# Kernel tuning notes

Measured on AMD Instinct MI355X. Metric: run time of the kernel, lower is better.

## Reference

```python
import jax, jax.numpy as jnp
import numpy as np
import math

B = 2048
INPUT_SIZE = 1024
OUTPUT_SIZE = 512
SPONGE = 1024
ACT = 256
REC = 256
STORE = ACT + REC  # 512
DEPTH = 8
BDEPTH = 10
NEUTRAL_C = 1.0
SQRT2 = math.sqrt(2.0)


def _make_structure():
    # Deterministic stand-in for the module's random.sample-based recall wiring.
    rng = np.random.RandomState(0)
    half = (SPONGE + 1) // 2
    shuffle_perm = np.array([i // 2 + (i % 2) * half for i in range(SPONGE)], dtype=np.int64)
    unused = []
    recall = []
    for i in range(DEPTH):
        unused.extend(range(i * STORE, (i + 1) * STORE))
        sel = rng.choice(len(unused), size=REC, replace=False)
        sel_set = set(sel.tolist())
        recall.append([unused[k] for k in sorted(sel_set)])
        unused = [u for k, u in enumerate(unused) if k not in sel_set]
    out_mem = np.array(sorted(unused), dtype=np.int64)  # 2048 leftover memory columns
    bf_size = len(out_mem) + SPONGE  # 3072
    bf_depth = int(math.ceil(math.log2(bf_size)))  # 12
    bf_half = (bf_size + 1) // 2
    bf_perm = np.array([i // 2 + (i % 2) * bf_half for i in range(bf_size)], dtype=np.int64)
    return shuffle_perm, np.array(recall, dtype=np.int64), out_mem, bf_perm, bf_size, bf_depth


def setup_inputs() -> dict:
    key = jax.random.key(0)
    ks = jax.random.split(key, 6)
    shuffle_perm, recall_idx, out_mem_idx, bf_perm, bf_size, bf_depth = _make_structure()
    return {
        "X": jax.random.normal(ks[0], (B, INPUT_SIZE), jnp.float32),
        "scales": jnp.ones((INPUT_SIZE,), jnp.float32),
        "angles": jax.random.uniform(ks[1], (DEPTH, BDEPTH, SPONGE // 2), jnp.float32) * (2 * math.pi),
        "act_bias": jax.random.normal(ks[2], (DEPTH, ACT), jnp.float32),
        "act_activation": jax.random.normal(ks[3], (DEPTH, ACT), jnp.float32),
        "act_curvature": jax.random.normal(ks[4], (DEPTH, ACT), jnp.float32),
        "bf_angles": jax.random.uniform(ks[5], (bf_depth, bf_size // 2), jnp.float32) * (2 * math.pi),
        "shuffle_perm": jnp.asarray(shuffle_perm),
        "recall_idx": jnp.asarray(recall_idx),
        "output_mem_idx": jnp.asarray(out_mem_idx),
        "bf_perm": jnp.asarray(bf_perm),
    }


def _base_activation(x, c):
    # In the source, `a` is overwritten with torch.tensor(1.0), so a == 1.
    t = (math.pi / 4) / c
    y0 = (1.0 / c) * (1.0 / SQRT2 - math.cos(math.pi / 2))  # = 1/(c*sqrt(2))
    m0 = math.sin(math.pi / 2)  # = 1
    y1 = (1.0 / c) * (1.0 / SQRT2 - 1.0)
    m1 = math.sin(0.0)  # = 0
    mid = (1.0 / c) * (1.0 / SQRT2 - jnp.cos(math.pi / 4 + c * x))
    return jnp.where(x > t, y0 + m0 * (x - t), jnp.where(x < -t, y1 + m1 * (x + t), mid))


def _butterfly(x, angles, perm):
    # angles: [n_layers, exch]; shuffle -> Givens rotation per pair, extra passthrough
    exch = angles.shape[1]
    for j in range(angles.shape[0]):
        s = x[:, perm]
        x1, x2 = s[:, :exch], s[:, exch:2 * exch]
        ca, sa = jnp.cos(angles[j]), jnp.sin(angles[j])
        x = jnp.concatenate([ca * x1 + sa * x2, -sa * x1 + ca * x2, s[:, 2 * exch:]], axis=1)
    return x


def reference(X, scales, angles, act_bias, act_activation, act_curvature, bf_angles,
              shuffle_perm, recall_idx, output_mem_idx, bf_perm):
    Xs = X * scales
    sponge = Xs[:, :SPONGE]  # input_size == sponge_size: no zero pad, memory[0] is empty
    mem = jnp.zeros((Xs.shape[0], DEPTH * STORE), Xs.dtype)
    for i in range(DEPTH):
        sponge = _butterfly(sponge, angles[i], shuffle_perm)
        x1 = sponge[:, STORE:STORE + ACT] + act_bias[i]  # activation_position == store_size
        c = 0.5 * NEUTRAL_C * (act_curvature[i] + jnp.sqrt(act_curvature[i] ** 2 + 1.0))
        ap = _base_activation(x1, c)
        am = _base_activation(-x1, c)
        act_out = jnp.stack([ap, am], axis=2).reshape(ap.shape[0], 2 * ACT)  # interleave +/-
        mem = mem.at[:, i * STORE:(i + 1) * STORE].set(sponge[:, :STORE])
        recall = mem[:, recall_idx[i]]  # indices only address already-filled columns
        # [act_out | sponge[store:act_pos] (empty) | sponge[act_pos+ACT:] | recall]
        sponge = jnp.concatenate([act_out, sponge[:, STORE + ACT:], recall], axis=1)
    pre = jnp.concatenate([mem[:, output_mem_idx], sponge], axis=1)  # [B, 3072]
    out = _butterfly(pre, bf_angles, bf_perm)
    return out[:, :OUTPUT_SIZE]
```

## Files before the change

kernel.cpp:

```cpp
#include <hip/hip_runtime.h>
#include <hip/hip_bf16.h>
#include <math.h>

#define NB 2048
#define DEPTH 8
#define BDEPTH 10
#define BFDEPTH 12

#define N_SPONGE_CS (DEPTH * BDEPTH * 512)
#define N_BF_CS     (BFDEPTH * 1536)
#define TAB_FLOATS  (2 * (N_SPONGE_CS + N_BF_CS))
#define MEM_FLOATS_PER_ROW 4096

__global__ void cs_precompute(const float* __restrict__ angles,
                              const float* __restrict__ bf_angles,
                              float* __restrict__ tab) {
    int i = blockIdx.x * 256 + threadIdx.x;
    float a;
    if (i < N_SPONGE_CS)                a = angles[i];
    else if (i < N_SPONGE_CS + N_BF_CS) a = bf_angles[i - N_SPONGE_CS];
    else return;
    float s, c;
    sincosf(a, &s, &c);
    tab[2 * i]     = c;
    tab[2 * i + 1] = s;
}

__device__ __forceinline__ float base_act(float x, float c, float ic, float tt,
                                          float y0, float y1) {
    float mid = ic * (0.70710678118654752f - __cosf(0.78539816339744831f + c * x));
    return x > tt ? (y0 + (x - tt)) : (x < -tt ? y1 : mid);
}

template <int MEM_LDS>
__launch_bounds__(256, 8)
__global__ void sponge_kernel(const float* __restrict__ X,
                              const float* __restrict__ scales,
                              const float* __restrict__ act_bias,
                              const float* __restrict__ act_curv,
                              const int*   __restrict__ recall_idx,
                              const int*   __restrict__ out_mem_idx,
                              const float* __restrict__ tab,
                              float*       __restrict__ gmem,
                              float*       __restrict__ out) {
    __shared__ float buf[3072];
    __shared__ __hip_bfloat16 memb[MEM_LDS ? 4096 : 2];
    const int t   = threadIdx.x;
    const int row = blockIdx.x;
    float* g = gmem + (size_t)row * MEM_FLOATS_PER_ROW;

    {
        float4 xv = ((const float4*)(X + (size_t)row * 1024))[t];
        float4 sv = ((const float4*)scales)[t];
        ((float4*)buf)[t] = make_float4(xv.x * sv.x, xv.y * sv.y,
                                        xv.z * sv.z, xv.w * sv.w);
    }
    __syncthreads();

    float* cur = buf;
    float* alt = buf + 1024;
    const float* tb = tab;

    for (int d = 0; d < DEPTH; ++d) {
        for (int st = 0; st < BDEPTH; ++st) {
            const float4 cs = *(const float4*)(tb + 4 * t);
            tb += 1024;
            float a = cur[t], b = cur[t + 256], c = cur[t + 512], e = cur[t + 768];
            ((float2*)(alt + 2 * t))[0] =
                make_float2( cs.x * a + cs.y * b,  cs.z * c + cs.w * e);
            ((float2*)(alt + 512 + 2 * t))[0] =
                make_float2(-cs.y * a + cs.x * b, -cs.w * c + cs.z * e);
            __syncthreads();
            float* tmp = cur; cur = alt; alt = tmp;
        }
        int ri = recall_idx[d * 256 + t];
        {
            float m0 = cur[t], m1 = cur[t + 256];
            if (MEM_LDS) {
                memb[d * 512 + t]       = __float2bfloat16(m0);
                memb[d * 512 + 256 + t] = __float2bfloat16(m1);
            } else {
                g[d * 512 + t]       = m0;
                g[d * 512 + 256 + t] = m1;
            }
        }
        {
            float x1 = cur[512 + t] + act_bias[d * 256 + t];
            float cu = act_curv[d * 256 + t];
            float c  = 0.5f * (cu + sqrtf(cu * cu + 1.0f));
            float ic = 1.0f / c;
            float tt = 0.78539816339744831f * ic;
            float y0 = 0.70710678118654752f * ic;
            float y1 = (0.70710678118654752f - 1.0f) * ic;
            float ap = base_act( x1, c, ic, tt, y0, y1);
            float am = base_act(-x1, c, ic, tt, y0, y1);
            ((float2*)(alt + 2 * t))[0] = make_float2(ap, am);
        }
        alt[512 + t] = cur[768 + t];
        __syncthreads();
        alt[768 + t] = MEM_LDS ? __bfloat162float(memb[ri]) : g[ri];
        __syncthreads();
        float* tmp = cur; cur = alt; alt = tmp;
    }

    float s0 = cur[t], s1 = cur[256 + t], s2 = cur[512 + t], s3 = cur[768 + t];
    __syncthreads();
    buf[2048 + t]       = s0;
    buf[2048 + 256 + t] = s1;
    buf[2048 + 512 + t] = s2;
    buf[2048 + 768 + t] = s3;
#pragma unroll
    for (int q = 0; q < 8; ++q) {
        int oi = out_mem_idx[q * 256 + t];
        buf[q * 256 + t] = MEM_LDS ? __bfloat162float(memb[oi]) : g[oi];
    }
    __syncthreads();

    const float* bft = tab + 2 * N_SPONGE_CS;

    for (int s = 0; s < 3; ++s) {
        const float* tbs = bft + s * 3072;
        float  r[12];
        float4 csg[3];
#pragma unroll
        for (int gi = 0; gi < 3; ++gi) {
            csg[gi] = *(const float4*)(tbs + 4 * t + 1024 * gi);
            r[4 * gi + 0] = buf[t + 256 * gi];
            r[4 * gi + 1] = buf[t + 256 * gi + 768];
            r[4 * gi + 2] = buf[t + 256 * gi + 1536];
            r[4 * gi + 3] = buf[t + 256 * gi + 2304];
        }
        __syncthreads();
#pragma unroll
        for (int gi = 0; gi < 3; ++gi) {
            int j0 = 2 * t + 512 * gi;
            float4 cs = csg[gi];
            float a = r[4 * gi], b = r[4 * gi + 1], c = r[4 * gi + 2], e = r[4 * gi + 3];
            ((float2*)(buf + j0))[0] =
                make_float2( cs.x * a + cs.y * b,  cs.z * c + cs.w * e);
            ((float2*)(buf + 1536 + j0))[0] =
                make_float2(-cs.y * a + cs.x * b, -cs.w * c + cs.z * e);
        }
        __syncthreads();
    }

#pragma unroll
    for (int s = 3; s < 11; ++s) {
        const float* tbs = bft + s * 3072;
        const int k = 10 - s;
        const int M = 768 >> k;
        const int Wl = 8 - k;
        const int Wm = (256 >> k) - 1;
        float  X1[2], X2[2];
        float2 cs2[2];
        int    pp[2];
#pragma unroll
        for (int u = 0; u < 2; ++u) {
            int i = t + 256 * u;
            int p = ((i >> Wl) * M) + (i & Wm);
            pp[u]  = p;
            cs2[u] = *(const float2*)(tbs + 2 * p);
            X1[u] = buf[(p >> 1) + (p & 1) * 1536];
            X2[u] = buf[768 + (p >> 1) + (p & 1) * 1536];
        }
        __syncthreads();
#pragma unroll
        for (int u = 0; u < 2; ++u) {
            buf[pp[u]]        =  cs2[u].x * X1[u] + cs2[u].y * X2[u];
            buf[pp[u] + 1536] = -cs2[u].y * X1[u] + cs2[u].x * X2[u];
        }
        __syncthreads();
    }

    {
        const float* tbs = bft + 11 * 3072;
        float4 cs = *(const float4*)(tbs + 4 * t);
        float a = buf[t], b = buf[768 + t], c = buf[1536 + t], e = buf[2304 + t];
        ((float2*)(out + (size_t)row * 512))[t] =
            make_float2(cs.x * a + cs.y * b, cs.z * c + cs.w * e);
    }
}

extern "C" void kernel_launch(void* const* d_in, const int* in_sizes, int n_in,
                              void* d_out, int out_size, void* d_ws, size_t ws_size,
                              hipStream_t stream) {
    const float* X          = (const float*)d_in[0];
    const float* scales     = (const float*)d_in[1];
    const float* angles     = (const float*)d_in[2];
    const float* act_bias   = (const float*)d_in[3];
    const float* act_curv   = (const float*)d_in[5];
    const float* bf_angles  = (const float*)d_in[6];
    const int*   recall_idx  = (const int*)d_in[8];
    const int*   out_mem_idx = (const int*)d_in[9];

    float* tab  = (float*)d_ws;
    float* gmem = (float*)d_ws + TAB_FLOATS;

    int total = N_SPONGE_CS + N_BF_CS;
    cs_precompute<<<(total + 255) / 256, 256, 0, stream>>>(angles, bf_angles, tab);

    size_t need = (size_t)TAB_FLOATS * 4 + (size_t)NB * MEM_FLOATS_PER_ROW * 4;
    if (ws_size >= need) {
        sponge_kernel<0><<<NB, 256, 0, stream>>>(X, scales, act_bias, act_curv,
                                                 recall_idx, out_mem_idx, tab,
                                                 gmem, (float*)d_out);
    } else {
        sponge_kernel<1><<<NB, 256, 0, stream>>>(X, scales, act_bias, act_curv,
                                                 recall_idx, out_mem_idx, tab,
                                                 gmem, (float*)d_out);
    }
}
```

Before: 133.5 us.

## Register-resident sponge butterflies with fused stage pairs and compacted LDS memory

Reworks the sponge phase so each thread holds four values in registers and applies two butterfly stages per LDS round trip. This halves the barriers and LDS traffic in the depth loop, using a precomputed, reordered cos/sin table. The per-row global memory scratch is replaced by a compacted fp32 LDS store, addressed through physical-slot index tables built in a separate precompute kernel. Activation constants are also precomputed. The cost is two extra small launches, more LDS per block, and more complex index arithmetic.

```diff
diff --git a/kernel.cpp b/kernel.cpp
--- a/kernel.cpp
+++ b/kernel.cpp
@@ -1,122 +1,194 @@
 #include <hip/hip_runtime.h>
-#include <hip/hip_bf16.h>
 #include <math.h>
 
 #define NB 2048
 #define DEPTH 8
-#define BDEPTH 10
-#define BFDEPTH 12
-
-#define N_SPONGE_CS (DEPTH * BDEPTH * 512)
-#define N_BF_CS     (BFDEPTH * 1536)
-#define TAB_FLOATS  (2 * (N_SPONGE_CS + N_BF_CS))
-#define MEM_FLOATS_PER_ROW 4096
-
-__global__ void cs_precompute(const float* __restrict__ angles,
-                              const float* __restrict__ bf_angles,
-                              float* __restrict__ tab) {
-    int i = blockIdx.x * 256 + threadIdx.x;
-    float a;
-    if (i < N_SPONGE_CS)                a = angles[i];
-    else if (i < N_SPONGE_CS + N_BF_CS) a = bf_angles[i - N_SPONGE_CS];
-    else return;
-    float s, c;
-    sincosf(a, &s, &c);
-    tab[2 * i]     = c;
-    tab[2 * i + 1] = s;
-}
-
-__device__ __forceinline__ float base_act(float x, float c, float ic, float tt,
-                                          float y0, float y1) {
-    float mid = ic * (0.70710678118654752f - __cosf(0.78539816339744831f + c * x));
+
+#define FTAB_OFF   0
+#define BFT_OFF    81920
+#define ACT4_OFF   118784
+#define PHYS_OFF   126976
+#define PHYSR_OFF  131072
+#define PHYSO_OFF  133120
+#define WS_FLOATS  135168
+
+__global__ void tab_precompute(const float* __restrict__ angles,
+                               const float* __restrict__ bf_angles,
+                               const float* __restrict__ act_bias,
+                               const float* __restrict__ act_curv,
+                               float* __restrict__ ws) {
+    int id = blockIdx.x * 256 + threadIdx.x;
+    if (id < 40960) {
+        int w  = id & 3;
+        int t  = (id >> 2) & 255;
+        int dg = id >> 10;
+        int d = dg / 5, g = dg - 5 * d;
+        int pA1 = 2 * (t & 127) + (t >> 7);
+        int pair = (w == 0) ? pA1 : (w == 1) ? (pA1 + 256)
+                 : (w == 2) ? (2 * pA1) : (2 * pA1 + 1);
+        int st = 2 * g + (w >> 1);
+        float a = angles[(d * 10 + st) * 512 + pair];
+        float s, c; sincosf(a, &s, &c);
+        ws[FTAB_OFF + 2 * id]     = c;
+        ws[FTAB_OFF + 2 * id + 1] = s;
+    } else if (id < 40960 + 18432) {
+        int idb = id - 40960;
+        float a = bf_angles[idb];
+        float s, c; sincosf(a, &s, &c);
+        ws[BFT_OFF + 2 * idb]     = c;
+        ws[BFT_OFF + 2 * idb + 1] = s;
+    } else if (id < 40960 + 18432 + 2048) {
+        int ida = id - 59392;
+        float cu = act_curv[ida];
+        float c  = 0.5f * (cu + sqrtf(cu * cu + 1.0f));
+        ((float4*)(ws + ACT4_OFF))[ida] =
+            make_float4(act_bias[ida], c, 1.0f / c, 0.0f);
+    }
+}
+
+__global__ void phys_precompute(const int* __restrict__ recall_idx,
+                                const int* __restrict__ out_mem_idx,
+                                float* __restrict__ ws) {
+    __shared__ int physL[4096];
+    int t = threadIdx.x;
+    for (int q = 0; q < 4; ++q) {
+        int v = t + q * 1024;
+        int p;
+        for (;;) {
+            int d = v >> 9, j = v & 511;
+            if (d == 0)  { p = j; break; }
+            if (j < 256) { p = 256 + d * 256 + j; break; }
+            v = recall_idx[(d - 1) * 256 + (j - 256)];
+        }
+        physL[t + q * 1024] = p;
+        ((int*)(ws + PHYS_OFF))[t + q * 1024] = p;
+    }
+    __syncthreads();
+    for (int q = 0; q < 2; ++q) {
+        int i = t + q * 1024;
+        ((int*)(ws + PHYSR_OFF))[i] = physL[recall_idx[i]];
+        ((int*)(ws + PHYSO_OFF))[i] = physL[out_mem_idx[i]];
+    }
+}
+
+__device__ __forceinline__ float actf(float x, float c, float ic) {
+    const float is2 = 0.70710678118654752f;
+    float tt = 0.78539816339744831f * ic;
+    float y0 = is2 * ic;
+    float y1 = (is2 - 1.0f) * ic;
+    float mid = ic * (is2 - __cosf(0.78539816339744831f + c * x));
     return x > tt ? (y0 + (x - tt)) : (x < -tt ? y1 : mid);
 }
 
-template <int MEM_LDS>
 __launch_bounds__(256, 8)
 __global__ void sponge_kernel(const float* __restrict__ X,
                               const float* __restrict__ scales,
-                              const float* __restrict__ act_bias,
-                              const float* __restrict__ act_curv,
-                              const int*   __restrict__ recall_idx,
-                              const int*   __restrict__ out_mem_idx,
-                              const float* __restrict__ tab,
-                              float*       __restrict__ gmem,
-                              float*       __restrict__ out) {
-    __shared__ float buf[3072];
-    __shared__ __hip_bfloat16 memb[MEM_LDS ? 4096 : 2];
+                              const float* __restrict__ ws,
+                              float* __restrict__ out) {
+    __shared__ float lds[4352];
+    float* memb = lds;
+    float* pb0  = lds + 2304;
+    float* pb1  = lds + 3328;
     const int t   = threadIdx.x;
     const int row = blockIdx.x;
-    float* g = gmem + (size_t)row * MEM_FLOATS_PER_ROW;
-
+
+    const float* ftab = ws + FTAB_OFF;
+    const float* bft  = ws + BFT_OFF;
+    const float4* act4 = (const float4*)(ws + ACT4_OFF);
+    const int* phys  = (const int*)(ws + PHYS_OFF);
+    const int* physr = (const int*)(ws + PHYSR_OFF);
+    const int* physo = (const int*)(ws + PHYSO_OFF);
+
+    const int tl = t & 127, th = t >> 7;
+    const int b  = tl + th * 512;
+    const int a  = 2 * tl + th;
+
+    float h0, h1, h2, h3;
     {
-        float4 xv = ((const float4*)(X + (size_t)row * 1024))[t];
-        float4 sv = ((const float4*)scales)[t];
-        ((float4*)buf)[t] = make_float4(xv.x * sv.x, xv.y * sv.y,
-                                        xv.z * sv.z, xv.w * sv.w);
-    }
+        const float* Xr = X + (size_t)row * 1024;
+        h0 = Xr[b]       * scales[b];
+        h1 = Xr[b + 128] * scales[b + 128];
+        h2 = Xr[b + 256] * scales[b + 256];
+        h3 = Xr[b + 384] * scales[b + 384];
+    }
+
+    float* wbuf = pb0;
+    float* rbuf = pb1;
+
+    for (int d = 0; d < DEPTH; ++d) {
+        for (int g = 0; g < 5; ++g) {
+            const float4* ft = (const float4*)(ftab + (size_t)((d * 5 + g) * 256 + t) * 8);
+            float4 csA = ft[0];
+            float4 csB = ft[1];
+            float g0 =  csA.x * h0 + csA.y * h2;
+            float g2 = -csA.y * h0 + csA.x * h2;
+            float g1 =  csA.z * h1 + csA.w * h3;
+            float g3 = -csA.w * h1 + csA.z * h3;
+            float f0 =  csB.x * g0 + csB.y * g1;
+            float f2 = -csB.y * g0 + csB.x * g1;
+            float f1 =  csB.z * g2 + csB.w * g3;
+            float f3 = -csB.w * g2 + csB.z * g3;
+            ((float2*)(wbuf + 2 * a))[0]       = make_float2(f0, f1);
+            ((float2*)(wbuf + 2 * a + 512))[0] = make_float2(f2, f3);
+            { float* tmp = wbuf; wbuf = rbuf; rbuf = tmp; }
+            __syncthreads();
+            if (g < 4) {
+                h0 = rbuf[b];
+                h1 = rbuf[b + 128];
+                h2 = rbuf[b + 256];
+                h3 = rbuf[b + 384];
+            }
+        }
+        const float* z = rbuf;
+        {
+            float2 mv = ((const float2*)(z + 2 * t))[0];
+            int2  pm  = ((const int2*)(phys + d * 512))[t];
+            memb[pm.x] = mv.x;
+            memb[pm.y] = mv.y;
+        }
+        int r0 = 0, r1 = 0;
+        if (t < 128) {
+            int k0 = t >> 1;
+            float x10 = z[512 + k0];
+            float x11 = z[512 + k0 + 64];
+            float x12 = z[512 + k0 + 128];
+            float x13 = z[512 + k0 + 192];
+            float4 a0 = act4[d * 256 + k0];
+            float4 a1 = act4[d * 256 + k0 + 64];
+            float4 a2 = act4[d * 256 + k0 + 128];
+            float4 a3 = act4[d * 256 + k0 + 192];
+            float sgn = (t & 1) ? -1.0f : 1.0f;
+            h0 = actf(sgn * (x10 + a0.x), a0.y, a0.z);
+            h1 = actf(sgn * (x11 + a1.x), a1.y, a1.z);
+            h2 = actf(sgn * (x12 + a2.x), a2.y, a2.z);
+            h3 = actf(sgn * (x13 + a3.x), a3.y, a3.z);
+        } else {
+            int u = t - 128;
+            h0 = z[768 + u];
+            h1 = z[896 + u];
+            r0 = physr[d * 256 + u];
+            r1 = physr[d * 256 + u + 128];
+        }
+        __syncthreads();
+        if (t >= 128) {
+            h2 = memb[r0];
+            h3 = memb[r1];
+        }
+    }
+
+    float gv[8];
+#pragma unroll
+    for (int q = 0; q < 8; ++q) gv[q] = memb[physo[q * 256 + t]];
     __syncthreads();
-
-    float* cur = buf;
-    float* alt = buf + 1024;
-    const float* tb = tab;
-
-    for (int d = 0; d < DEPTH; ++d) {
-        for (int st = 0; st < BDEPTH; ++st) {
-            const float4 cs = *(const float4*)(tb + 4 * t);
-            tb += 1024;
-            float a = cur[t], b = cur[t + 256], c = cur[t + 512], e = cur[t + 768];
-            ((float2*)(alt + 2 * t))[0] =
-                make_float2( cs.x * a + cs.y * b,  cs.z * c + cs.w * e);
-            ((float2*)(alt + 512 + 2 * t))[0] =
-                make_float2(-cs.y * a + cs.x * b, -cs.w * c + cs.z * e);
-            __syncthreads();
-            float* tmp = cur; cur = alt; alt = tmp;
-        }
-        int ri = recall_idx[d * 256 + t];
-        {
-            float m0 = cur[t], m1 = cur[t + 256];
-            if (MEM_LDS) {
-                memb[d * 512 + t]       = __float2bfloat16(m0);
-                memb[d * 512 + 256 + t] = __float2bfloat16(m1);
-            } else {
-                g[d * 512 + t]       = m0;
-                g[d * 512 + 256 + t] = m1;
-            }
-        }
-        {
-            float x1 = cur[512 + t] + act_bias[d * 256 + t];
-            float cu = act_curv[d * 256 + t];
-            float c  = 0.5f * (cu + sqrtf(cu * cu + 1.0f));
-            float ic = 1.0f / c;
-            float tt = 0.78539816339744831f * ic;
-            float y0 = 0.70710678118654752f * ic;
-            float y1 = (0.70710678118654752f - 1.0f) * ic;
-            float ap = base_act( x1, c, ic, tt, y0, y1);
-            float am = base_act(-x1, c, ic, tt, y0, y1);
-            ((float2*)(alt + 2 * t))[0] = make_float2(ap, am);
-        }
-        alt[512 + t] = cur[768 + t];
-        __syncthreads();
-        alt[768 + t] = MEM_LDS ? __bfloat162float(memb[ri]) : g[ri];
-        __syncthreads();
-        float* tmp = cur; cur = alt; alt = tmp;
-    }
-
-    float s0 = cur[t], s1 = cur[256 + t], s2 = cur[512 + t], s3 = cur[768 + t];
+#pragma unroll
+    for (int q = 0; q < 8; ++q) lds[q * 256 + t] = gv[q];
+    lds[2048 + b]       = h0;
+    lds[2048 + b + 128] = h1;
+    lds[2048 + b + 256] = h2;
+    lds[2048 + b + 384] = h3;
     __syncthreads();
-    buf[2048 + t]       = s0;
-    buf[2048 + 256 + t] = s1;
-    buf[2048 + 512 + t] = s2;
-    buf[2048 + 768 + t] = s3;
-#pragma unroll
-    for (int q = 0; q < 8; ++q) {
-        int oi = out_mem_idx[q * 256 + t];
-        buf[q * 256 + t] = MEM_LDS ? __bfloat162float(memb[oi]) : g[oi];
-    }
-    __syncthreads();
-
-    const float* bft = tab + 2 * N_SPONGE_CS;
+
+    float* buf = lds;
 
     for (int s = 0; s < 3; ++s) {
         const float* tbs = bft + s * 3072;
@@ -135,11 +207,11 @@
         for (int gi = 0; gi < 3; ++gi) {
             int j0 = 2 * t + 512 * gi;
             float4 cs = csg[gi];
-            float a = r[4 * gi], b = r[4 * gi + 1], c = r[4 * gi + 2], e = r[4 * gi + 3];
+            float av = r[4 * gi], bv = r[4 * gi + 1], cv = r[4 * gi + 2], ev = r[4 * gi + 3];
             ((float2*)(buf + j0))[0] =
-                make_float2( cs.x * a + cs.y * b,  cs.z * c + cs.w * e);
+                make_float2( cs.x * av + cs.y * bv,  cs.z * cv + cs.w * ev);
             ((float2*)(buf + 1536 + j0))[0] =
-                make_float2(-cs.y * a + cs.x * b, -cs.w * c + cs.z * e);
+                make_float2(-cs.y * av + cs.x * bv, -cs.w * cv + cs.z * ev);
         }
         __syncthreads();
     }
@@ -147,8 +219,8 @@
 #pragma unroll
     for (int s = 3; s < 11; ++s) {
         const float* tbs = bft + s * 3072;
-        const int k = 10 - s;
-        const int M = 768 >> k;
+        const int k  = 10 - s;
+        const int M  = 768 >> k;
         const int Wl = 8 - k;
         const int Wm = (256 >> k) - 1;
         float  X1[2], X2[2];
@@ -175,9 +247,9 @@
     {
         const float* tbs = bft + 11 * 3072;
         float4 cs = *(const float4*)(tbs + 4 * t);
-        float a = buf[t], b = buf[768 + t], c = buf[1536 + t], e = buf[2304 + t];
+        float av = buf[t], bv = buf[768 + t], cv = buf[1536 + t], ev = buf[2304 + t];
         ((float2*)(out + (size_t)row * 512))[t] =
-            make_float2(cs.x * a + cs.y * b, cs.z * c + cs.w * e);
+            make_float2(cs.x * av + cs.y * bv, cs.z * cv + cs.w * ev);
     }
 }
 
@@ -193,20 +265,9 @@
     const int*   recall_idx  = (const int*)d_in[8];
     const int*   out_mem_idx = (const int*)d_in[9];
 
-    float* tab  = (float*)d_ws;
-    float* gmem = (float*)d_ws + TAB_FLOATS;
-
-    int total = N_SPONGE_CS + N_BF_CS;
-    cs_precompute<<<(total + 255) / 256, 256, 0, stream>>>(angles, bf_angles, tab);
-
-    size_t need = (size_t)TAB_FLOATS * 4 + (size_t)NB * MEM_FLOATS_PER_ROW * 4;
-    if (ws_size >= need) {
-        sponge_kernel<0><<<NB, 256, 0, stream>>>(X, scales, act_bias, act_curv,
-                                                 recall_idx, out_mem_idx, tab,
-                                                 gmem, (float*)d_out);
-    } else {
-        sponge_kernel<1><<<NB, 256, 0, stream>>>(X, scales, act_bias, act_curv,
-                                                 recall_idx, out_mem_idx, tab,
-                                                 gmem, (float*)d_out);
-    }
-}
+    float* ws = (float*)d_ws;
+
+    tab_precompute<<<240, 256, 0, stream>>>(angles, bf_angles, act_bias, act_curv, ws);
+    phys_precompute<<<1, 1024, 0, stream>>>(recall_idx, out_mem_idx, ws);
+    sponge_kernel<<<NB, 256, 0, stream>>>(X, scales, ws, (float*)d_out);
+}
```

New measurement: 127.0 us. 4.8% less time.
